# Performance work log

Measured on AMD Instinct MI355X. Metric: run time of the kernel, lower is better.

Reference implementation:

```python
import jax, jax.numpy as jnp
import numpy as np

WEIGHT = 10.0
# illegal[i, j] == True  iff transition (i -> j) is illegal; from {(0,2),(1,0),(2,0),(2,1)}
_ILLEGAL = np.zeros((3, 3), dtype=bool)
for _i, _j in [(0, 2), (1, 0), (2, 0), (2, 1)]:
    _ILLEGAL[_i, _j] = True


def setup_inputs() -> dict:
    key = jax.random.key(0)
    phase_logits = jax.random.normal(key, (2048, 8192, 3), dtype=jnp.float32)
    return {"phase_logits": phase_logits}


def reference(phase_logits):
    B, T, C = phase_logits.shape
    illegal = jnp.asarray(_ILLEGAL)
    pred = jnp.argmax(phase_logits, axis=-1)          # [B, T]
    pt = pred[:, :-1]                                  # phase at t     [B, T-1]
    pt1 = pred[:, 1:]                                  # phase at t+1   [B, T-1]
    mask = illegal[pt, pt1]                            # [B, T-1] bool
    # logit of the (argmax) illegal phase at t+1: phase_logits[b, t+1, pt1]
    gathered = jnp.take_along_axis(phase_logits[:, 1:, :], pt1[..., None], axis=-1)[..., 0]
    loss = jnp.sum(jnp.where(mask, gathered * gathered, jnp.zeros_like(gathered)))
    count = jnp.sum(mask.astype(phase_logits.dtype))
    return jnp.where(count > 0, WEIGHT * loss / count, jnp.zeros_like(loss))
```

## Files before the change

### kernel.cpp

```cpp
#include <hip/hip_runtime.h>


#define TLEN      8192
#define CPR_SHIFT 11
#define CPR_MASK  2047u
#define NTHREADS  256
#define KCHUNK    8

__device__ __forceinline__ void argmax3(float a, float b, float c, int& bi, float& bm) {
    bm = a; bi = 0;
    if (b > bm) { bm = b; bi = 1; }
    if (c > bm) { bm = c; bi = 2; }
}

__global__ __launch_bounds__(NTHREADS) void pcl_main(const float* __restrict__ x,
                                                     float* __restrict__ part_loss,
                                                     unsigned int* __restrict__ part_cnt) {
    const unsigned int gsz = gridDim.x * NTHREADS;
    const unsigned int gid = blockIdx.x * NTHREADS + threadIdx.x;
    const int lane = threadIdx.x & 63;

    float loss = 0.0f;
    unsigned int cnt = 0;

    #pragma unroll
    for (int j = 0; j < KCHUNK; ++j) {
        unsigned int c   = gid + (unsigned int)j * gsz;
        unsigned int row = c >> CPR_SHIFT;
        unsigned int s4  = c & CPR_MASK;
        const float4* p = (const float4*)(x + ((size_t)row * TLEN + (s4 << 2)) * 3);

        float4 f0 = p[0];
        float4 f1 = p[1];
        float4 f2 = p[2];

        float v[4][3] = {
            {f0.x, f0.y, f0.z},
            {f0.w, f1.x, f1.y},
            {f1.z, f1.w, f2.x},
            {f2.y, f2.z, f2.w}
        };

        int   idx[4];
        float mx[4];
        #pragma unroll
        for (int k = 0; k < 4; ++k) argmax3(v[k][0], v[k][1], v[k][2], idx[k], mx[k]);

        int   nidx = __shfl_down(idx[0], 1, 64);
        float nmx  = __shfl_down(mx[0], 1, 64);
        if (lane == 63 && s4 != CPR_MASK) {
            float4 f3 = p[3];
            argmax3(f3.x, f3.y, f3.z, nidx, nmx);
        }

        #pragma unroll
        for (int k = 0; k < 3; ++k) {
            int code = idx[k] * 3 + idx[k + 1];
            if ((0xCC >> code) & 1) { loss = fmaf(mx[k + 1], mx[k + 1], loss); cnt++; }
        }
        if (s4 != CPR_MASK) {
            int code = idx[3] * 3 + nidx;
            if ((0xCC >> code) & 1) { loss = fmaf(nmx, nmx, loss); cnt++; }
        }
    }

    #pragma unroll
    for (int off = 32; off > 0; off >>= 1) {
        loss += __shfl_down(loss, off, 64);
        cnt  += __shfl_down(cnt,  off, 64);
    }

    __shared__ float        sl[4];
    __shared__ unsigned int sc[4];
    int wid = threadIdx.x >> 6;
    if (lane == 0) { sl[wid] = loss; sc[wid] = cnt; }
    __syncthreads();

    if (threadIdx.x == 0) {
        part_loss[blockIdx.x] = sl[0] + sl[1] + sl[2] + sl[3];
        part_cnt[blockIdx.x]  = sc[0] + sc[1] + sc[2] + sc[3];
    }
}

__global__ __launch_bounds__(NTHREADS) void pcl_final(const float* __restrict__ part_loss,
                                                      const unsigned int* __restrict__ part_cnt,
                                                      float* __restrict__ out, int npart) {
    double L = 0.0;
    unsigned int C = 0;
    for (int i = threadIdx.x; i < npart; i += NTHREADS) {
        L += (double)part_loss[i];
        C += part_cnt[i];
    }
    #pragma unroll
    for (int off = 32; off > 0; off >>= 1) {
        L += __shfl_down(L, off, 64);
        C += __shfl_down(C, off, 64);
    }
    __shared__ double       sl[4];
    __shared__ unsigned int sc[4];
    int lane = threadIdx.x & 63;
    int wid  = threadIdx.x >> 6;
    if (lane == 0) { sl[wid] = L; sc[wid] = C; }
    __syncthreads();
    if (threadIdx.x == 0) {
        double       Lt = sl[0] + sl[1] + sl[2] + sl[3];
        unsigned int Ct = sc[0] + sc[1] + sc[2] + sc[3];
        out[0] = (Ct > 0u) ? (float)(10.0 * Lt / (double)Ct) : 0.0f;
    }
}

extern "C" void kernel_launch(void* const* d_in, const int* in_sizes, int n_in,
                              void* d_out, int out_size, void* d_ws, size_t ws_size,
                              hipStream_t stream) {
    const float* x = (const float*)d_in[0];
    const int B = in_sizes[0] / (3 * TLEN);

    const int grid = B;

    float*        part_loss = (float*)d_ws;
    unsigned int* part_cnt  = (unsigned int*)((char*)d_ws + (size_t)grid * sizeof(float));

    pcl_main<<<grid, NTHREADS, 0, stream>>>(x, part_loss, part_cnt);
    pcl_final<<<1, NTHREADS, 0, stream>>>(part_loss, part_cnt, (float*)d_out, grid);
}
```

Before: 272.9 us.

## Switch to one timestep per thread with hoisted 12-byte loads and packed argmax

```diff
diff --git a/kernel.cpp b/kernel.cpp
--- a/kernel.cpp
+++ b/kernel.cpp
@@ -2,65 +2,75 @@
 
 
 #define TLEN      8192
-#define CPR_SHIFT 11
-#define CPR_MASK  2047u
+#define TMASK     8191u
 #define NTHREADS  256
-#define KCHUNK    8
+#define KCH       8
+#define NBLK      8192
 
-__device__ __forceinline__ void argmax3(float a, float b, float c, int& bi, float& bm) {
-    bm = a; bi = 0;
-    if (b > bm) { bm = b; bi = 1; }
-    if (c > bm) { bm = c; bi = 2; }
+struct alignas(4) F3 { float a, b, c; };
+
+__device__ __forceinline__ F3 load_f3(const float* __restrict__ p) {
+    F3 v;
+    __builtin_memcpy(&v, p, sizeof(F3));
+    return v;
+}
+
+__device__ __forceinline__ int argmax3_pack(F3 v) {
+    float bm = v.a; int bi = 0;
+    if (v.b > bm) { bm = v.b; bi = 1; }
+    if (v.c > bm) { bm = v.c; bi = 2; }
+    return (__float_as_int(bm) & ~3) | bi;
 }
 
 __global__ __launch_bounds__(NTHREADS) void pcl_main(const float* __restrict__ x,
                                                      float* __restrict__ part_loss,
-                                                     unsigned int* __restrict__ part_cnt) {
-    const unsigned int gsz = gridDim.x * NTHREADS;
+                                                     unsigned int* __restrict__ part_cnt,
+                                                     unsigned int total) {
+    const unsigned int gsz = NBLK * NTHREADS;
     const unsigned int gid = blockIdx.x * NTHREADS + threadIdx.x;
     const int lane = threadIdx.x & 63;
 
+    F3 own[KCH];
+    #pragma unroll
+    for (int j = 0; j < KCH; ++j) {
+        unsigned int c = gid + (unsigned int)j * gsz;
+        own[j] = load_f3(x + (size_t)3 * c);
+    }
+
+    F3 nbv[KCH];
+    if (lane == 63) {
+        #pragma unroll
+        for (int j = 0; j < KCH; ++j) {
+            unsigned int s = gid + (unsigned int)j * gsz + 1u;
+            if (s >= total) s = total - 1u;
+            nbv[j] = load_f3(x + (size_t)3 * s);
+        }
+    }
+
+    int pk[KCH];
+    #pragma unroll
+    for (int j = 0; j < KCH; ++j) pk[j] = argmax3_pack(own[j]);
+
+    int fb[KCH] = {};
+    if (lane == 63) {
+        #pragma unroll
+        for (int j = 0; j < KCH; ++j) fb[j] = argmax3_pack(nbv[j]);
+    }
+
     float loss = 0.0f;
     unsigned int cnt = 0;
-
     #pragma unroll
-    for (int j = 0; j < KCHUNK; ++j) {
-        unsigned int c   = gid + (unsigned int)j * gsz;
-        unsigned int row = c >> CPR_SHIFT;
-        unsigned int s4  = c & CPR_MASK;
-        const float4* p = (const float4*)(x + ((size_t)row * TLEN + (s4 << 2)) * 3);
-
-        float4 f0 = p[0];
-        float4 f1 = p[1];
-        float4 f2 = p[2];
-
-        float v[4][3] = {
-            {f0.x, f0.y, f0.z},
-            {f0.w, f1.x, f1.y},
-            {f1.z, f1.w, f2.x},
-            {f2.y, f2.z, f2.w}
-        };
-
-        int   idx[4];
-        float mx[4];
-        #pragma unroll
-        for (int k = 0; k < 4; ++k) argmax3(v[k][0], v[k][1], v[k][2], idx[k], mx[k]);
-
-        int   nidx = __shfl_down(idx[0], 1, 64);
-        float nmx  = __shfl_down(mx[0], 1, 64);
-        if (lane == 63 && s4 != CPR_MASK) {
-            float4 f3 = p[3];
-            argmax3(f3.x, f3.y, f3.z, nidx, nmx);
-        }
-
-        #pragma unroll
-        for (int k = 0; k < 3; ++k) {
-            int code = idx[k] * 3 + idx[k + 1];
-            if ((0xCC >> code) & 1) { loss = fmaf(mx[k + 1], mx[k + 1], loss); cnt++; }
-        }
-        if (s4 != CPR_MASK) {
-            int code = idx[3] * 3 + nidx;
-            if ((0xCC >> code) & 1) { loss = fmaf(nmx, nmx, loss); cnt++; }
+    for (int j = 0; j < KCH; ++j) {
+        unsigned int c = gid + (unsigned int)j * gsz;
+        int npk = __shfl_down(pk[j], 1, 64);
+        if (lane == 63) npk = fb[j];
+        if ((c & TMASK) != TMASK) {
+            int code = (pk[j] & 3) * 3 + (npk & 3);
+            if ((0xCC >> code) & 1) {
+                float nmx = __int_as_float(npk & ~3);
+                loss = fmaf(nmx, nmx, loss);
+                cnt++;
+            }
         }
     }
 
@@ -113,13 +123,11 @@
                               void* d_out, int out_size, void* d_ws, size_t ws_size,
                               hipStream_t stream) {
     const float* x = (const float*)d_in[0];
-    const int B = in_sizes[0] / (3 * TLEN);
-
-    const int grid = B;
+    const unsigned int total = (unsigned int)(in_sizes[0] / 3);
 
     float*        part_loss = (float*)d_ws;
-    unsigned int* part_cnt  = (unsigned int*)((char*)d_ws + (size_t)grid * sizeof(float));
+    unsigned int* part_cnt  = (unsigned int*)((char*)d_ws + (size_t)NBLK * sizeof(float));
 
-    pcl_main<<<grid, NTHREADS, 0, stream>>>(x, part_loss, part_cnt);
-    pcl_final<<<1, NTHREADS, 0, stream>>>(part_loss, part_cnt, (float*)d_out, grid);
+    pcl_main<<<NBLK, NTHREADS, 0, stream>>>(x, part_loss, part_cnt, total);
+    pcl_final<<<1, NTHREADS, 0, stream>>>(part_loss, part_cnt, (float*)d_out, NBLK);
 }
```

New measurement: 276.4 us. No clear change (+1.3%).
